# Kernel tuning notes

Measured on AMD Instinct MI355X. Metric: run time of the kernel, lower is better.

The kernel has to match this reference:

```python
import jax, jax.numpy as jnp
import numpy as np

# Dimensions from init_kwargs
B, C, H, W = 128, 3, 64, 64
K, S, P = 5, 2, 2            # kernel, stride, padding
OC = 64                      # base_channels
OH = (H + 2 * P - K) // S + 1  # 32
OW = (W + 2 * P - K) // S + 1  # 32
FC_IN = OC * OH * OW         # 65536
HID = 24 * OC                # 1536
NCLS = 10
EPS = 1e-5                   # BatchNorm eps (torch default)


def setup_inputs() -> dict:
    key = jax.random.key(0)
    ks = jax.random.split(key, 4)
    x = jax.random.normal(ks[0], (B, C, H, W), dtype=jnp.float32)
    # LocallyConnected2d: unshared weight per output location [OC, C*K*K, OH, OW]
    lc_w = jax.random.normal(ks[1], (OC, C * K * K, OH, OW), dtype=jnp.float32) * 0.05
    bn1_g = jnp.ones((OC,), jnp.float32)
    bn1_b = jnp.zeros((OC,), jnp.float32)
    fc1_w = jax.random.normal(ks[2], (HID, FC_IN), dtype=jnp.float32) * 0.01
    bn2_g = jnp.ones((HID,), jnp.float32)
    bn2_b = jnp.zeros((HID,), jnp.float32)
    fc2_w = jax.random.normal(ks[3], (NCLS, HID), dtype=jnp.float32) * 0.02
    return {"x": x, "lc_w": lc_w, "bn1_g": bn1_g, "bn1_b": bn1_b,
            "fc1_w": fc1_w, "bn2_g": bn2_g, "bn2_b": bn2_b, "fc2_w": fc2_w}


def reference(x, lc_w, bn1_g, bn1_b, fc1_w, bn2_g, bn2_b, fc2_w):
    # --- LocallyConnected2d (no bias): unfold + per-location contraction ---
    # patches: [B, C*K*K, OH, OW]
    patches = jax.lax.conv_general_dilated_patches(
        x, filter_shape=(K, K), window_strides=(S, S),
        padding=((P, P), (P, P)))
    out = jnp.einsum('bphw,ophw->bohw', patches, lc_w)  # [B, OC, OH, OW]

    # --- BatchNorm2d (training mode: batch stats, biased var) + ReLU ---
    mean = out.mean(axis=(0, 2, 3))
    var = out.var(axis=(0, 2, 3))
    out = (out - mean[None, :, None, None]) * jax.lax.rsqrt(var + EPS)[None, :, None, None]
    out = out * bn1_g[None, :, None, None] + bn1_b[None, :, None, None]
    out = jax.nn.relu(out)

    # --- Classifier: Linear -> BN1d -> ReLU -> Linear ---
    h = out.reshape(B, -1) @ fc1_w.T  # [B, HID]
    m2 = h.mean(axis=0)
    v2 = h.var(axis=0)
    h = (h - m2) * jax.lax.rsqrt(v2 + EPS) * bn2_g + bn2_b
    h = jax.nn.relu(h)
    return h @ fc2_w.T  # [B, NCLS]
```

## Files before the change

### kernel.cpp

```cpp
#include <hip/hip_runtime.h>
#include <hip/hip_bf16.h>
#include <stdint.h>

#define B_   128
#define C_   3
#define H_   64
#define W_   64
#define KS   5
#define OC   64
#define OH   32
#define OW   32
#define PSZ  75
#define FCIN 65536
#define HID  1536
#define NCLS 10
#define EPSV 1e-5f

typedef __attribute__((ext_vector_type(8))) short  bf16x8;
typedef __attribute__((ext_vector_type(8))) short  short8;
typedef __attribute__((ext_vector_type(4))) float  f32x4;

static __device__ __forceinline__ float bf2f(short u) {
  union { unsigned int i; float f; } v;
  v.i = ((unsigned int)(unsigned short)u) << 16;
  return v.f;
}
static __device__ __forceinline__ short f2bf(float f) {
  union { float f; unsigned int i; } v; v.f = f;
  unsigned int r = v.i + 0x7FFF + ((v.i >> 16) & 1);
  return (short)(r >> 16);
}
static __device__ __forceinline__ float u2f(unsigned int u) {
  union { unsigned int i; float f; } v; v.i = u; return v.f;
}

static __device__ __forceinline__ void gld16(const unsigned short* g, unsigned short* l) {
  __builtin_amdgcn_global_load_lds(
      (const __attribute__((address_space(1))) unsigned int*)g,
      (__attribute__((address_space(3))) unsigned int*)l, 16, 0, 0);
}
static __device__ __forceinline__ void gld16f(const float* g, float* l) {
  __builtin_amdgcn_global_load_lds(
      (const __attribute__((address_space(1))) unsigned int*)g,
      (__attribute__((address_space(3))) unsigned int*)l, 16, 0, 0);
}

__global__ __launch_bounds__(256, 2) void k1_conv(
    const float* __restrict__ x, const float* __restrict__ lcw,
    unsigned short* __restrict__ outb) {
  const int h  = blockIdx.x;
  const int og = blockIdx.y;
  const int zb = blockIdx.z;
  const int tid = threadIdx.x;
  const int w  = tid & 31;
  const int ot = tid >> 5;
  const int o0 = og * 16 + ot * 2;

  __shared__ unsigned short xs[16][C_][KS][72];

  const int row0 = 2 * h - 2;
  for (int g = 0; g < 2; ++g) {
    const int bg = zb * 2 + g;
    if (g) __syncthreads();

    if (tid < 240) {
      int t = tid;
      int r = t % KS;  t /= KS;
      int c = t % C_;
      int b = t / C_;
      *(unsigned int*)&xs[b][c][r][0]  = 0u;
      *(unsigned int*)&xs[b][c][r][66] = 0u;
      *(unsigned int*)&xs[b][c][r][68] = 0u;
      *(unsigned int*)&xs[b][c][r][70] = 0u;
    }
    for (int v = tid; v < 16 * C_ * KS * 16; v += 256) {
      int col4 = v & 15;
      int t    = v >> 4;
      int r    = t % KS;  t /= KS;
      int c    = t % C_;
      int b    = t / C_;
      int grow = row0 + r;
      f32x4 val = (f32x4){0.f, 0.f, 0.f, 0.f};
      if ((unsigned)grow < 64u)
        val = *(const f32x4*)&x[(((long)(bg * 16 + b) * C_ + c) * 64 + grow) * 64 + col4 * 4];
      unsigned int p0 = ((unsigned int)(unsigned short)f2bf(val[0])) |
                        (((unsigned int)(unsigned short)f2bf(val[1])) << 16);
      unsigned int p1 = ((unsigned int)(unsigned short)f2bf(val[2])) |
                        (((unsigned int)(unsigned short)f2bf(val[3])) << 16);
      *(unsigned int*)&xs[b][c][r][2 + col4 * 4]     = p0;
      *(unsigned int*)&xs[b][c][r][2 + col4 * 4 + 2] = p1;
    }
    __syncthreads();

    float acc[2][16];
    #pragma unroll
    for (int oo = 0; oo < 2; ++oo)
      #pragma unroll
      for (int b = 0; b < 16; ++b) acc[oo][b] = 0.f;

    #pragma unroll 1
    for (int c = 0; c < C_; ++c) {
      #pragma unroll 1
      for (int kh = 0; kh < KS; ++kh) {
        float wA[KS], wB[KS];
        const float* wpA = lcw + ((long)o0 * PSZ + c * 25 + kh * 5) * 1024 + h * 32 + w;
        const float* wpB = wpA + (long)PSZ * 1024;
        #pragma unroll
        for (int p = 0; p < KS; ++p) {
          wA[p] = wpA[(long)p * 1024];
          wB[p] = wpB[(long)p * 1024];
        }
        #pragma unroll
        for (int b = 0; b < 16; ++b) {
          const unsigned int* rowp = (const unsigned int*)&xs[b][c][kh][0];
          unsigned int d0 = rowp[w];
          unsigned int d1 = rowp[w + 1];
          unsigned int d2 = rowp[w + 2];
          float v0 = u2f(d0 << 16), v1 = u2f(d0 & 0xffff0000u);
          float v2 = u2f(d1 << 16), v3 = u2f(d1 & 0xffff0000u);
          float v4 = u2f(d2 << 16);
          acc[0][b] += wA[0] * v0 + wA[1] * v1 + wA[2] * v2 + wA[3] * v3 + wA[4] * v4;
          acc[1][b] += wB[0] * v0 + wB[1] * v1 + wB[2] * v2 + wB[3] * v3 + wB[4] * v4;
        }
      }
    }

    #pragma unroll
    for (int oo = 0; oo < 2; ++oo)
      #pragma unroll
      for (int b = 0; b < 16; ++b)
        outb[((long)(bg * 16 + b) * OC + (o0 + oo)) * 1024 + h * 32 + w] =
            (unsigned short)f2bf(acc[oo][b]);
  }
}

__global__ __launch_bounds__(1024) void k2_stats(
    const unsigned short* __restrict__ outb,
    const float* __restrict__ g, const float* __restrict__ bta,
    float* __restrict__ sc, float* __restrict__ sh) {
  const int o = blockIdx.x;
  const int tid = threadIdx.x;
  float s = 0.f, s2 = 0.f;
  const int i8 = (tid & 127) * 8;
  const int bsub = tid >> 7;
  for (int pass = 0; pass < 16; ++pass) {
    int b = bsub + pass * 8;
    const short8 v = *(const short8*)(outb + (((long)b * OC + o) << 10) + i8);
    #pragma unroll
    for (int j = 0; j < 8; ++j) { float f = bf2f(v[j]); s += f; s2 += f * f; }
  }
  #pragma unroll
  for (int off = 32; off; off >>= 1) {
    s  += __shfl_down(s, off);
    s2 += __shfl_down(s2, off);
  }
  __shared__ float ls[16], ls2[16];
  int wid = tid >> 6;
  if ((tid & 63) == 0) { ls[wid] = s; ls2[wid] = s2; }
  __syncthreads();
  if (tid == 0) {
    float ts = 0.f, ts2 = 0.f;
    for (int i = 0; i < 16; ++i) { ts += ls[i]; ts2 += ls2[i]; }
    const float inv = 1.0f / (float)(B_ * 1024);
    float mean = ts * inv;
    float var  = ts2 * inv - mean * mean;
    float rstd = 1.0f / sqrtf(var + EPSV);
    float scv  = g[o] * rstd;
    sc[o] = scv;
    sh[o] = bta[o] - mean * scv;
  }
}

__global__ __launch_bounds__(256) void k25_pack(
    const unsigned short* __restrict__ outb,
    const float* __restrict__ sc, const float* __restrict__ sh,
    unsigned short* __restrict__ ab) {
  const int c = blockIdx.x * 256 + threadIdx.x;
  const int l15 = c & 15;
  const int lq  = (c >> 4) & 3;
  const int mf  = (c >> 6) & 7;
  const int kb  = c >> 9;
  const int m   = mf * 16 + l15;
  const int k   = kb * 32 + lq * 8;
  const int o   = k >> 10;
  const int hw  = k & 1023;
  float scv = sc[o], shv = sh[o];
  short8 v = *(const short8*)(outb + ((long)m * 64 + o) * 1024 + hw);
  short8 r;
  #pragma unroll
  for (int j = 0; j < 8; ++j) {
    float f = bf2f(v[j]) * scv + shv;
    r[j] = f2bf(fmaxf(f, 0.f));
  }
  *(short8*)(ab + (long)c * 8) = r;
}

__global__ __launch_bounds__(256, 3) void k3_gemm(
    const unsigned short* __restrict__ ab, const float* __restrict__ w1,
    float* __restrict__ part, int ksteps, int splits) {
  const int nwg = 24 * splits;
  const int chunk = nwg >> 3;
  const int bid = blockIdx.x;
  const int lid = (bid & 7) * chunk + (bid >> 3);
  const int split = lid / 24;
  const int ntile = lid % 24;

  const int tid  = threadIdx.x;
  const int lane = tid & 63;
  const int wid  = tid >> 6;
  const int n0   = ntile * 64 + wid * 16;
  const int l15  = lane & 15;
  const int lq   = lane >> 4;

  __shared__ unsigned short sa[3][4096];
  __shared__ float sw[3][4][512];

  const int kb0 = split * ksteps;
  const int kmask = ksteps - 1;
  const int phase = (lid * 29) & kmask;
  const long wsrc = (long)(n0 + l15) * FCIN + (long)kb0 * 32 + lq * 8;
  const int last = ksteps - 1;

#define STAGE(T, BUF) do {                                                   \
    int Tp = ((T) + phase) & kmask;                                          \
    long gb = ((long)(kb0 + Tp) * 512 + wid * 128) * 8;                      \
    unsigned short* lb = &sa[BUF][wid * 1024];                               \
    gld16(ab + gb + (long)lane * 8, lb);                                     \
    gld16(ab + gb + 512 + (long)lane * 8, lb + 512);                         \
    const float* wg = w1 + wsrc + (long)Tp * 32;                             \
    float* wlb = &sw[BUF][wid][0];                                           \
    gld16f(wg, wlb);                                                         \
    gld16f(wg + 4, wlb + 256);                                               \
  } while (0)

#define COMPUTE(X) do {                                                      \
    f32x4 wv0 = *(const f32x4*)&sw[X][wid][lane * 4];                        \
    f32x4 wv1 = *(const f32x4*)&sw[X][wid][256 + lane * 4];                  \
    bf16x8 bfr;                                                              \
    _Pragma("unroll")                                                        \
    for (int j = 0; j < 4; ++j) bfr[j] = f2bf(wv0[j]);                       \
    _Pragma("unroll")                                                        \
    for (int j = 0; j < 4; ++j) bfr[4 + j] = f2bf(wv1[j]);                   \
    __builtin_amdgcn_s_setprio(1);                                           \
    _Pragma("unroll")                                                        \
    for (int m = 0; m < 8; ++m) {                                            \
      bf16x8 afr = *(const bf16x8*)(&sa[X][m * 512 + lane * 8]);             \
      acc[m] = __builtin_amdgcn_mfma_f32_16x16x32_bf16(afr, bfr, acc[m], 0, 0, 0); \
    }                                                                        \
    __builtin_amdgcn_s_setprio(0);                                           \
  } while (0)

  f32x4 acc[8];
  #pragma unroll
  for (int m = 0; m < 8; ++m) acc[m] = (f32x4){0.f, 0.f, 0.f, 0.f};

  STAGE(0, 0);
  STAGE((1 <= last ? 1 : last), 1);

  for (int t = 0; t < ksteps; ++t) {
    asm volatile("s_waitcnt vmcnt(4)" ::: "memory");
    __builtin_amdgcn_sched_barrier(0);
    __builtin_amdgcn_s_barrier();
    __builtin_amdgcn_sched_barrier(0);
    int tn = (t + 2 <= last) ? (t + 2) : last;
    STAGE(tn, (t + 2) % 3);
    COMPUTE(t % 3);
  }
#undef STAGE
#undef COMPUTE

  float* pp = part + (long)split * (B_ * HID);
  #pragma unroll
  for (int m = 0; m < 8; ++m) {
    int row = m * 16 + lq * 4;
    #pragma unroll
    for (int r = 0; r < 4; ++r)
      pp[(long)(row + r) * HID + n0 + l15] = acc[m][r];
  }
}

__global__ __launch_bounds__(256) void k4_bn2(
    const float* __restrict__ part, const float* __restrict__ g2,
    const float* __restrict__ b2, float* __restrict__ h2, int splits) {
  const int nb = blockIdx.x;
  const int tid = threadIdx.x;
  const int nl = tid & 3;
  const int bt = tid >> 2;
  const int n  = nb * 4 + nl;

  float h0 = 0.f, h1 = 0.f;
  for (int s = 0; s < splits; ++s) {
    const float* pp = part + (long)s * (B_ * HID) + n;
    h0 += pp[(long)bt * HID];
    h1 += pp[(long)(bt + 64) * HID];
  }
  float s1 = h0 + h1, s2v = h0 * h0 + h1 * h1;

  __shared__ float r1[256], r2[256];
  r1[tid] = s1; r2[tid] = s2v;
  __syncthreads();
  for (int off = 32; off; off >>= 1) {
    if (bt < off) { r1[tid] += r1[tid + off * 4]; r2[tid] += r2[tid + off * 4]; }
    __syncthreads();
  }
  __shared__ float scs[4], shs[4];
  if (bt == 0) {
    float mean = r1[nl] * (1.0f / 128.f);
    float var  = r2[nl] * (1.0f / 128.f) - mean * mean;
    float rstd = 1.0f / sqrtf(var + EPSV);
    float sc = g2[n] * rstd;
    scs[nl] = sc; shs[nl] = b2[n] - mean * sc;
  }
  __syncthreads();
  float sc = scs[nl], shf = shs[nl];
  h2[(long)bt * HID + n]        = fmaxf(h0 * sc + shf, 0.f);
  h2[(long)(bt + 64) * HID + n] = fmaxf(h1 * sc + shf, 0.f);
}

__global__ __launch_bounds__(256) void k5_fc2(
    const float* __restrict__ h2, const float* __restrict__ w2,
    float* __restrict__ out) {
  const int b = blockIdx.x;
  const int tid = threadIdx.x;
  float acc[NCLS];
  #pragma unroll
  for (int c = 0; c < NCLS; ++c) acc[c] = 0.f;
  for (int n = tid; n < HID; n += 256) {
    float hvv = h2[(long)b * HID + n];
    #pragma unroll
    for (int c = 0; c < NCLS; ++c) acc[c] += hvv * w2[c * HID + n];
  }
  #pragma unroll
  for (int off = 32; off; off >>= 1)
    #pragma unroll
    for (int c = 0; c < NCLS; ++c) acc[c] += __shfl_down(acc[c], off);
  __shared__ float ls[4][NCLS];
  int wid = tid >> 6;
  if ((tid & 63) == 0)
    for (int c = 0; c < NCLS; ++c) ls[wid][c] = acc[c];
  __syncthreads();
  if (tid < NCLS)
    out[b * NCLS + tid] = ls[0][tid] + ls[1][tid] + ls[2][tid] + ls[3][tid];
}

extern "C" void kernel_launch(void* const* d_in, const int* in_sizes, int n_in,
                              void* d_out, int out_size, void* d_ws, size_t ws_size,
                              hipStream_t stream) {
  const float* x    = (const float*)d_in[0];
  const float* lcw  = (const float*)d_in[1];
  const float* bn1g = (const float*)d_in[2];
  const float* bn1b = (const float*)d_in[3];
  const float* fc1w = (const float*)d_in[4];
  const float* bn2g = (const float*)d_in[5];
  const float* bn2b = (const float*)d_in[6];
  const float* fc2w = (const float*)d_in[7];
  float* out = (float*)d_out;

  char* ws = (char*)d_ws;
  unsigned short* outb = (unsigned short*)(ws);
  unsigned short* ab   = (unsigned short*)(ws + (size_t)16 * 1024 * 1024);
  float* sc1 = (float*)(ws + (size_t)32 * 1024 * 1024);
  float* sh1 = sc1 + 64;
  size_t base = (size_t)32 * 1024 * 1024 + 4096;
  float* part = (float*)(ws + base);

  int splits = 32;
  size_t h2need = (size_t)B_ * HID * 4;
  while (splits > 4 && base + (size_t)splits * B_ * HID * 4 + h2need > ws_size)
    splits >>= 1;
  float* h2 = (float*)(ws + base + (size_t)splits * B_ * HID * 4);

  k1_conv<<<dim3(32, 4, 4), 256, 0, stream>>>(x, lcw, outb);
  k2_stats<<<64, 1024, 0, stream>>>(outb, bn1g, bn1b, sc1, sh1);
  k25_pack<<<4096, 256, 0, stream>>>(outb, sc1, sh1, ab);
  int ksteps = FCIN / splits / 32;
  k3_gemm<<<24 * splits, 256, 0, stream>>>(ab, fc1w, part, ksteps, splits);
  k4_bn2<<<384, 256, 0, stream>>>(part, bn2g, bn2b, h2, splits);
  k5_fc2<<<128, 256, 0, stream>>>(h2, fc2w, out);
}
```

Baseline: 209.6 us.

## Widen FC1 GEMM N-tile to 128 and double split-K to cut activation re-reads

Result: slower. 258.4 us (+23.3%).

```diff
diff --git a/kernel.cpp b/kernel.cpp
--- a/kernel.cpp
+++ b/kernel.cpp
@@ -195,78 +195,102 @@
   *(short8*)(ab + (long)c * 8) = r;
 }
 
-__global__ __launch_bounds__(256, 3) void k3_gemm(
+__global__ __launch_bounds__(256, 2) void k3_gemm(
     const unsigned short* __restrict__ ab, const float* __restrict__ w1,
     float* __restrict__ part, int ksteps, int splits) {
-  const int nwg = 24 * splits;
+  const int nwg = 12 * splits;
   const int chunk = nwg >> 3;
   const int bid = blockIdx.x;
   const int lid = (bid & 7) * chunk + (bid >> 3);
-  const int split = lid / 24;
-  const int ntile = lid % 24;
+  const int split = lid / 12;
+  const int ntile = lid % 12;
 
   const int tid  = threadIdx.x;
   const int lane = tid & 63;
   const int wid  = tid >> 6;
-  const int n0   = ntile * 64 + wid * 16;
+  const int n0   = ntile * 128 + wid * 16;
   const int l15  = lane & 15;
   const int lq   = lane >> 4;
 
-  __shared__ unsigned short sa[3][4096];
-  __shared__ float sw[3][4][512];
+  __shared__ unsigned short sa[2][4096];
+  __shared__ float sw[3][2][4][512];
 
   const int kb0 = split * ksteps;
   const int kmask = ksteps - 1;
   const int phase = (lid * 29) & kmask;
-  const long wsrc = (long)(n0 + l15) * FCIN + (long)kb0 * 32 + lq * 8;
+  const long wsrc0 = (long)(n0 + l15) * FCIN + (long)kb0 * 32 + lq * 8;
+  const long wsrc1 = wsrc0 + (long)64 * FCIN;
   const int last = ksteps - 1;
 
-#define STAGE(T, BUF) do {                                                   \
+#define STAGE_A(T, BUF) do {                                                 \
     int Tp = ((T) + phase) & kmask;                                          \
     long gb = ((long)(kb0 + Tp) * 512 + wid * 128) * 8;                      \
     unsigned short* lb = &sa[BUF][wid * 1024];                               \
     gld16(ab + gb + (long)lane * 8, lb);                                     \
     gld16(ab + gb + 512 + (long)lane * 8, lb + 512);                         \
-    const float* wg = w1 + wsrc + (long)Tp * 32;                             \
-    float* wlb = &sw[BUF][wid][0];                                           \
-    gld16f(wg, wlb);                                                         \
-    gld16f(wg + 4, wlb + 256);                                               \
   } while (0)
 
-#define COMPUTE(X) do {                                                      \
-    f32x4 wv0 = *(const f32x4*)&sw[X][wid][lane * 4];                        \
-    f32x4 wv1 = *(const f32x4*)&sw[X][wid][256 + lane * 4];                  \
-    bf16x8 bfr;                                                              \
-    _Pragma("unroll")                                                        \
-    for (int j = 0; j < 4; ++j) bfr[j] = f2bf(wv0[j]);                       \
-    _Pragma("unroll")                                                        \
-    for (int j = 0; j < 4; ++j) bfr[4 + j] = f2bf(wv1[j]);                   \
+#define STAGE_W(T, BUF) do {                                                 \
+    int Tp = ((T) + phase) & kmask;                                          \
+    const float* wg0 = w1 + wsrc0 + (long)Tp * 32;                           \
+    const float* wg1 = w1 + wsrc1 + (long)Tp * 32;                           \
+    float* wl0 = &sw[BUF][0][wid][0];                                        \
+    float* wl1 = &sw[BUF][1][wid][0];                                        \
+    gld16f(wg0, wl0);                                                        \
+    gld16f(wg0 + 4, wl0 + 256);                                              \
+    gld16f(wg1, wl1);                                                        \
+    gld16f(wg1 + 4, wl1 + 256);                                              \
+  } while (0)
+
+#define COMPUTE(XW, XA) do {                                                 \
+    bf16x8 bfr0, bfr1;                                                       \
+    {                                                                        \
+      f32x4 a0 = *(const f32x4*)&sw[XW][0][wid][lane * 4];                   \
+      f32x4 a1 = *(const f32x4*)&sw[XW][0][wid][256 + lane * 4];             \
+      _Pragma("unroll")                                                      \
+      for (int j = 0; j < 4; ++j) { bfr0[j] = f2bf(a0[j]); bfr0[4 + j] = f2bf(a1[j]); } \
+    }                                                                        \
+    {                                                                        \
+      f32x4 a0 = *(const f32x4*)&sw[XW][1][wid][lane * 4];                   \
+      f32x4 a1 = *(const f32x4*)&sw[XW][1][wid][256 + lane * 4];             \
+      _Pragma("unroll")                                                      \
+      for (int j = 0; j < 4; ++j) { bfr1[j] = f2bf(a0[j]); bfr1[4 + j] = f2bf(a1[j]); } \
+    }                                                                        \
     __builtin_amdgcn_s_setprio(1);                                           \
     _Pragma("unroll")                                                        \
     for (int m = 0; m < 8; ++m) {                                            \
-      bf16x8 afr = *(const bf16x8*)(&sa[X][m * 512 + lane * 8]);             \
-      acc[m] = __builtin_amdgcn_mfma_f32_16x16x32_bf16(afr, bfr, acc[m], 0, 0, 0); \
+      bf16x8 afr = *(const bf16x8*)(&sa[XA][m * 512 + lane * 8]);            \
+      acc[m][0] = __builtin_amdgcn_mfma_f32_16x16x32_bf16(afr, bfr0, acc[m][0], 0, 0, 0); \
+      acc[m][1] = __builtin_amdgcn_mfma_f32_16x16x32_bf16(afr, bfr1, acc[m][1], 0, 0, 0); \
     }                                                                        \
     __builtin_amdgcn_s_setprio(0);                                           \
   } while (0)
 
-  f32x4 acc[8];
-  #pragma unroll
-  for (int m = 0; m < 8; ++m) acc[m] = (f32x4){0.f, 0.f, 0.f, 0.f};
-
-  STAGE(0, 0);
-  STAGE((1 <= last ? 1 : last), 1);
+  f32x4 acc[8][2];
+  #pragma unroll
+  for (int m = 0; m < 8; ++m) {
+    acc[m][0] = (f32x4){0.f, 0.f, 0.f, 0.f};
+    acc[m][1] = (f32x4){0.f, 0.f, 0.f, 0.f};
+  }
+
+  STAGE_A(0, 0);
+  STAGE_W(0, 0);
+  STAGE_W((1 <= last ? 1 : last), 1);
 
   for (int t = 0; t < ksteps; ++t) {
     asm volatile("s_waitcnt vmcnt(4)" ::: "memory");
     __builtin_amdgcn_sched_barrier(0);
     __builtin_amdgcn_s_barrier();
     __builtin_amdgcn_sched_barrier(0);
-    int tn = (t + 2 <= last) ? (t + 2) : last;
-    STAGE(tn, (t + 2) % 3);
-    COMPUTE(t % 3);
-  }
-#undef STAGE
+    int ta = (t + 1 <= last) ? (t + 1) : last;
+    int tw = (t + 2 <= last) ? (t + 2) : last;
+    STAGE_A(ta, (t + 1) & 1);
+    STAGE_W(tw, (t + 2) % 3);
+    COMPUTE(t % 3, t & 1);
+  }
+  asm volatile("s_waitcnt vmcnt(0)" ::: "memory");
+#undef STAGE_A
+#undef STAGE_W
 #undef COMPUTE
 
   float* pp = part + (long)split * (B_ * HID);
@@ -274,8 +298,12 @@
   for (int m = 0; m < 8; ++m) {
     int row = m * 16 + lq * 4;
     #pragma unroll
-    for (int r = 0; r < 4; ++r)
-      pp[(long)(row + r) * HID + n0 + l15] = acc[m][r];
+    for (int g = 0; g < 2; ++g) {
+      int col = n0 + g * 64 + l15;
+      #pragma unroll
+      for (int r = 0; r < 4; ++r)
+        pp[(long)(row + r) * HID + col] = acc[m][g][r];
+    }
   }
 }
 
@@ -364,7 +392,7 @@
   size_t base = (size_t)32 * 1024 * 1024 + 4096;
   float* part = (float*)(ws + base);
 
-  int splits = 32;
+  int splits = 64;
   size_t h2need = (size_t)B_ * HID * 4;
   while (splits > 4 && base + (size_t)splits * B_ * HID * 4 + h2need > ws_size)
     splits >>= 1;
@@ -374,7 +402,7 @@
   k2_stats<<<64, 1024, 0, stream>>>(outb, bn1g, bn1b, sc1, sh1);
   k25_pack<<<4096, 256, 0, stream>>>(outb, sc1, sh1, ab);
   int ksteps = FCIN / splits / 32;
-  k3_gemm<<<24 * splits, 256, 0, stream>>>(ab, fc1w, part, ksteps, splits);
+  k3_gemm<<<12 * splits, 256, 0, stream>>>(ab, fc1w, part, ksteps, splits);
   k4_bn2<<<384, 256, 0, stream>>>(part, bn2g, bn2b, h2, splits);
   k5_fc2<<<128, 256, 0, stream>>>(h2, fc2w, out);
 }
```
